# Optimization experiments

Hardware: AMD Instinct MI355X
Metric: run time of the kernel (lower is better)

Reference implementation:

```python
import jax, jax.numpy as jnp
import numpy as np

INPUT_DIM = 1024
OUTPUT_DIM = 1024
DEGREE = 8


def setup_inputs() -> dict:
    key = jax.random.key(0)
    k1, k2 = jax.random.split(key)
    x = jax.random.normal(k1, (8192, INPUT_DIM), dtype=jnp.float32)
    std = 1.0 / (INPUT_DIM * (DEGREE + 1))
    cheby_coeffs = jax.random.normal(k2, (INPUT_DIM, OUTPUT_DIM, DEGREE + 1), dtype=jnp.float32) * std
    return {"x": x, "cheby_coeffs": cheby_coeffs}


def reference(x, cheby_coeffs):
    # x: [B, I]; cheby_coeffs: [I, O, D+1]
    degree = cheby_coeffs.shape[-1] - 1
    t = jnp.clip(jnp.tanh(x), -0.999, 0.999)            # [B, I]
    theta = jnp.arccos(t)[..., None]                     # [B, I, 1]
    arange = jnp.arange(degree + 1, dtype=x.dtype)       # [D+1]
    basis = jnp.cos(theta * arange)                      # [B, I, D+1] Chebyshev T_d(t)
    y = jnp.einsum('bid,iod->bo', basis, cheby_coeffs)   # [B, O]
    return y
```

## Files before the change

### kernel.cpp

```cpp
#include <hip/hip_runtime.h>
#include <stdint.h>

#define B_ROWS 8192
#define I_DIM  1024
#define N_DIM  1024
#define NDEG   9
#define K_DIM  (I_DIM * (NDEG-1))

#define BM 256
#define BN 128
#define BK 64
#define NT (K_DIM / BK)

typedef __attribute__((ext_vector_type(8)))  short short8;
typedef __attribute__((ext_vector_type(16))) float f32x16;

__device__ __forceinline__ unsigned short f2bf(float f) {
  union { float f; uint32_t u; } v; v.f = f;
  uint32_t u = v.u;
  u += 0x7FFFu + ((u >> 16) & 1u);
  return (unsigned short)(u >> 16);
}

__device__ __forceinline__ float bf2f(unsigned short h) {
  union { uint32_t u; float f; } v; v.u = ((uint32_t)h) << 16;
  return v.f;
}

__device__ __forceinline__ uint32_t pk_bf16(float lo, float hi) {
  uint32_t r;
  asm("v_cvt_pk_bf16_f32 %0, %1, %2" : "=v"(r) : "v"(lo), "v"(hi));
  return r;
}

__device__ __forceinline__ float fast_tanh(float x) {
  float e = __expf(2.0f * x);
  return 1.0f - __fdividef(2.0f, e + 1.0f);
}

__device__ __forceinline__ int h2(int r) { return (r >> 2) & 7; }

__global__ __launch_bounds__(256) void repack_kernel(const float* __restrict__ cf,
                                                     unsigned short* __restrict__ Bt,
                                                     float* __restrict__ bias) {
  __shared__ unsigned short L[32][584];
  const int i0  = blockIdx.x * 32;
  const int o0  = blockIdx.y * 64;
  const int tid = threadIdx.x;

  #pragma unroll
  for (int j = 0; j < 18; ++j) {
    const int f4  = j * 256 + tid;
    const int il  = f4 / 144;
    const int odq = f4 % 144;
    const float4 v = *reinterpret_cast<const float4*>(
        cf + ((size_t)(i0 + il) * N_DIM + o0) * NDEG + (size_t)odq * 4);
    ushort4 w;
    w.x = f2bf(v.x); w.y = f2bf(v.y); w.z = f2bf(v.z); w.w = f2bf(v.w);
    *reinterpret_cast<ushort4*>(&L[il][odq * 4]) = w;
  }
  __syncthreads();

  const int o  = tid >> 2;
  const int ci = tid & 3;
  const size_t base = (size_t)(o0 + o) * K_DIM + (size_t)(i0 + ci * 8) * 8;
  #pragma unroll
  for (int p = 0; p < 8; ++p) {
    const int il = ci * 8 + p;
    uint4 u;
    u.x = (uint32_t)L[il][o*9 + 1] | ((uint32_t)L[il][o*9 + 2] << 16);
    u.y = (uint32_t)L[il][o*9 + 3] | ((uint32_t)L[il][o*9 + 4] << 16);
    u.z = (uint32_t)L[il][o*9 + 5] | ((uint32_t)L[il][o*9 + 6] << 16);
    u.w = (uint32_t)L[il][o*9 + 7] | ((uint32_t)L[il][o*9 + 8] << 16);
    *reinterpret_cast<uint4*>(Bt + base + (size_t)p * 8) = u;
  }
  if (tid < 64) {
    float s = 0.f;
    #pragma unroll
    for (int il = 0; il < 32; ++il) s += bf2f(L[il][tid * 9]);
    atomicAdd(&bias[o0 + tid], s);
  }
}

__global__ __launch_bounds__(512, 2) void gemm_kernel(const float* __restrict__ x,
                                                      const unsigned short* __restrict__ Bt,
                                                      const float* __restrict__ bias,
                                                      float* __restrict__ C) {
  extern __shared__ unsigned short sm[];
  const int tid  = threadIdx.x;
  const int lane = tid & 63;
  const int wave = tid >> 6;
  const int l31  = lane & 31;
  const int half = lane >> 5;
  const int wm   = wave >> 1;
  const int wn   = wave & 1;

  const int bid = blockIdx.x;
  const int mt  = (bid & 7) + 8 * (bid >> 6);
  const int nt  = (bid >> 3) & 7;
  const int m0  = mt * BM;
  const int n0  = nt * BN;

  const int sr   = tid >> 3;
  const int slot = tid & 7;

  const unsigned short* Bbase = Bt + (size_t)n0 * K_DIM;

  f32x16 acc[2][2];
  #pragma unroll
  for (int a = 0; a < 2; ++a)
    #pragma unroll
    for (int b = 0; b < 2; ++b)
      #pragma unroll
      for (int r = 0; r < 16; ++r)
        acc[a][b][r] = 0.f;

#define STAGE_B(s, bf, kk) { const int r_ = (s)*64 + sr; const int gc_ = slot ^ h2(r_);     \
    __builtin_amdgcn_global_load_lds(                                                       \
        (const __attribute__((address_space(1))) void*)(Bbase + (size_t)r_*K_DIM + (kk) + gc_*8), \
        (__attribute__((address_space(3))) void*)&sm[32768 + (bf)*8192 + r_*64 + slot*8], 16, 0, 0); }

#define LOADX(xr, tt) {                                                                     \
    _Pragma("unroll")                                                                       \
    for (int q = 0; q < 4; ++q)                                                             \
      xr[q] = x[(size_t)(m0 + q*64 + sr) * I_DIM + (tt)*8 + slot]; }

#define BASIS(bf, xr) {                                                                     \
    _Pragma("unroll")                                                                       \
    for (int q = 0; q < 4; ++q) {                                                           \
      const int r_ = q*64 + sr;                                                             \
      float t = fast_tanh(xr[q]);                                                           \
      t = fminf(fmaxf(t, -0.999f), 0.999f);                                                 \
      const float t2 = t + t;                                                               \
      const float T1 = t;                                                                   \
      const float T2 = t2*t - 1.0f;                                                         \
      const float T3 = t2*T2 - T1;                                                          \
      const float T4 = t2*T3 - T2;                                                          \
      const float T5 = t2*T4 - T3;                                                          \
      const float T6 = t2*T5 - T4;                                                          \
      const float T7 = t2*T6 - T5;                                                          \
      const float T8 = t2*T7 - T6;                                                          \
      uint4 u;                                                                              \
      u.x = pk_bf16(T1, T2); u.y = pk_bf16(T3, T4);                                         \
      u.z = pk_bf16(T5, T6); u.w = pk_bf16(T7, T8);                                         \
      *reinterpret_cast<uint4*>(&sm[(bf)*16384 + r_*64 + ((slot ^ h2(r_)))*8]) = u;         \
    } }

  { STAGE_B(0, 0, 0) STAGE_B(1, 0, 0) }
  float xr[4];
  LOADX(xr, 0)
  BASIS(0, xr)
  __syncthreads();

  const int rowA0 = wm * 64 + l31;
  const int rowA1 = wm * 64 + 32 + l31;
  const int rowB0 = wn * 64 + l31;
  const int rowB1 = wn * 64 + 32 + l31;
  const int hA0 = h2(rowA0), hA1 = h2(rowA1), hB0 = h2(rowB0), hB1 = h2(rowB1);

  for (int kt = 0; kt < NT; ++kt) {
    const int  cur  = kt & 1;
    const int  nxt  = cur ^ 1;
    const bool more = (kt + 1 < NT);
    const unsigned short* Asc = &sm[cur * 16384];
    const unsigned short* Bsc = &sm[32768 + cur * 8192];

    if (more) { STAGE_B(0, nxt, (kt + 1) * BK) STAGE_B(1, nxt, (kt + 1) * BK) LOADX(xr, kt + 1) }
    __builtin_amdgcn_sched_barrier(0);

    short8 av[2][4], bv[2][4];
#define READ4(ks) {                                                                          \
    const int c_ = (ks) * 2 + half;                                                          \
    av[0][ks] = *reinterpret_cast<const short8*>(&Asc[rowA0 * 64 + (c_ ^ hA0) * 8]);         \
    av[1][ks] = *reinterpret_cast<const short8*>(&Asc[rowA1 * 64 + (c_ ^ hA1) * 8]);         \
    bv[0][ks] = *reinterpret_cast<const short8*>(&Bsc[rowB0 * 64 + (c_ ^ hB0) * 8]);         \
    bv[1][ks] = *reinterpret_cast<const short8*>(&Bsc[rowB1 * 64 + (c_ ^ hB1) * 8]); }

    READ4(0)
    #pragma unroll
    for (int ks = 0; ks < 4; ++ks) {
      if (ks < 3) READ4(ks + 1)
      acc[0][0] = __builtin_amdgcn_mfma_f32_32x32x16_bf16(av[0][ks], bv[0][ks], acc[0][0], 0, 0, 0);
      acc[0][1] = __builtin_amdgcn_mfma_f32_32x32x16_bf16(av[0][ks], bv[1][ks], acc[0][1], 0, 0, 0);
      acc[1][0] = __builtin_amdgcn_mfma_f32_32x32x16_bf16(av[1][ks], bv[0][ks], acc[1][0], 0, 0, 0);
      acc[1][1] = __builtin_amdgcn_mfma_f32_32x32x16_bf16(av[1][ks], bv[1][ks], acc[1][1], 0, 0, 0);
      if (ks < 3) __builtin_amdgcn_sched_group_barrier(0x100, 4, 0);
      __builtin_amdgcn_sched_group_barrier(0x008, 4, 0);
    }
#undef READ4

    __builtin_amdgcn_sched_barrier(0);
    if (more) BASIS(nxt, xr)

    __syncthreads();
  }
#undef STAGE_B
#undef LOADX
#undef BASIS

  #pragma unroll
  for (int ni = 0; ni < 2; ++ni) {
    const int col  = n0 + wn * 64 + ni * 32 + l31;
    const float bc = bias[col];
    #pragma unroll
    for (int mi = 0; mi < 2; ++mi) {
      const int rbase = m0 + wm * 64 + mi * 32 + 4 * half;
      #pragma unroll
      for (int r = 0; r < 16; ++r) {
        const int row = rbase + (r & 3) + 8 * (r >> 2);
        C[(size_t)row * N_DIM + col] = acc[mi][ni][r] + bc;
      }
    }
  }
}

extern "C" void kernel_launch(void* const* d_in, const int* in_sizes, int n_in,
                              void* d_out, int out_size, void* d_ws, size_t ws_size,
                              hipStream_t stream) {
  const float* x      = (const float*)d_in[0];
  const float* coeffs = (const float*)d_in[1];
  float* y            = (float*)d_out;

  const size_t bt_bytes = (size_t)N_DIM * K_DIM * sizeof(unsigned short);
  unsigned short* Bt = (unsigned short*)d_ws;
  float* bias        = (float*)((char*)d_ws + bt_bytes);

  hipMemsetAsync(bias, 0, N_DIM * sizeof(float), stream);

  hipFuncSetAttribute((const void*)gemm_kernel,
                      hipFuncAttributeMaxDynamicSharedMemorySize, 98304);

  repack_kernel<<<dim3(I_DIM / 32, N_DIM / 64), 256, 0, stream>>>(coeffs, Bt, bias);
  gemm_kernel<<<(B_ROWS / BM) * (N_DIM / BN), 512, 98304, stream>>>(x, Bt, bias, y);
}
```

Baseline: 293.7 us.

## Interleave basis computation with MFMAs and prefetch x two tiles ahead

Restructures the main K loop: it is manually unrolled by two, and x values are double-buffered in registers and loaded two tiles ahead. The Chebyshev basis computation for the next A tile is split per row group and interleaved between the MFMA groups through sched_group_barrier, rather than run after all MFMAs. __syncthreads is replaced by explicit vmcnt/lgkmcnt waits plus s_barrier, and LDS write offsets and x pointers are precomputed. The aim is to hide the VALU basis math and global-load latency behind matrix ops, at the cost of more registers and fragile hand-written wait counts.

```diff
diff --git a/kernel.cpp b/kernel.cpp
--- a/kernel.cpp
+++ b/kernel.cpp
@@ -106,6 +106,15 @@
 
   const unsigned short* Bbase = Bt + (size_t)n0 * K_DIM;
 
+  int awoff[4];
+  const float* xptr[4];
+  #pragma unroll
+  for (int q = 0; q < 4; ++q) {
+    const int r_ = q * 64 + sr;
+    awoff[q] = r_ * 64 + (slot ^ h2(r_)) * 8;
+    xptr[q]  = x + (size_t)(m0 + r_) * I_DIM + slot;
+  }
+
   f32x16 acc[2][2];
   #pragma unroll
   for (int a = 0; a < 2; ++a)
@@ -122,14 +131,10 @@
 
 #define LOADX(xr, tt) {                                                                     \
     _Pragma("unroll")                                                                       \
-    for (int q = 0; q < 4; ++q)                                                             \
-      xr[q] = x[(size_t)(m0 + q*64 + sr) * I_DIM + (tt)*8 + slot]; }
-
-#define BASIS(bf, xr) {                                                                     \
-    _Pragma("unroll")                                                                       \
-    for (int q = 0; q < 4; ++q) {                                                           \
-      const int r_ = q*64 + sr;                                                             \
-      float t = fast_tanh(xr[q]);                                                           \
+    for (int q = 0; q < 4; ++q) xr[q] = xptr[q][(tt) * 8]; }
+
+#define BASIS_Q(bf, q, xv) {                                                                \
+      float t = fast_tanh(xv);                                                              \
       t = fminf(fmaxf(t, -0.999f), 0.999f);                                                 \
       const float t2 = t + t;                                                               \
       const float T1 = t;                                                                   \
@@ -143,14 +148,7 @@
       uint4 u;                                                                              \
       u.x = pk_bf16(T1, T2); u.y = pk_bf16(T3, T4);                                         \
       u.z = pk_bf16(T5, T6); u.w = pk_bf16(T7, T8);                                         \
-      *reinterpret_cast<uint4*>(&sm[(bf)*16384 + r_*64 + ((slot ^ h2(r_)))*8]) = u;         \
-    } }
-
-  { STAGE_B(0, 0, 0) STAGE_B(1, 0, 0) }
-  float xr[4];
-  LOADX(xr, 0)
-  BASIS(0, xr)
-  __syncthreads();
+      *reinterpret_cast<uint4*>(&sm[(bf)*16384 + awoff[q]]) = u; }
 
   const int rowA0 = wm * 64 + l31;
   const int rowA1 = wm * 64 + 32 + l31;
@@ -158,45 +156,91 @@
   const int rowB1 = wn * 64 + 32 + l31;
   const int hA0 = h2(rowA0), hA1 = h2(rowA1), hB0 = h2(rowB0), hB1 = h2(rowB1);
 
-  for (int kt = 0; kt < NT; ++kt) {
-    const int  cur  = kt & 1;
-    const int  nxt  = cur ^ 1;
-    const bool more = (kt + 1 < NT);
-    const unsigned short* Asc = &sm[cur * 16384];
-    const unsigned short* Bsc = &sm[32768 + cur * 8192];
-
-    if (more) { STAGE_B(0, nxt, (kt + 1) * BK) STAGE_B(1, nxt, (kt + 1) * BK) LOADX(xr, kt + 1) }
-    __builtin_amdgcn_sched_barrier(0);
-
-    short8 av[2][4], bv[2][4];
-#define READ4(ks) {                                                                          \
+#define READ4(Asc, Bsc, av, bv, ks) {                                                        \
     const int c_ = (ks) * 2 + half;                                                          \
     av[0][ks] = *reinterpret_cast<const short8*>(&Asc[rowA0 * 64 + (c_ ^ hA0) * 8]);         \
     av[1][ks] = *reinterpret_cast<const short8*>(&Asc[rowA1 * 64 + (c_ ^ hA1) * 8]);         \
     bv[0][ks] = *reinterpret_cast<const short8*>(&Bsc[rowB0 * 64 + (c_ ^ hB0) * 8]);         \
     bv[1][ks] = *reinterpret_cast<const short8*>(&Bsc[rowB1 * 64 + (c_ ^ hB1) * 8]); }
 
-    READ4(0)
+#define MFMA4(av, bv, ks)                                                                    \
+    acc[0][0] = __builtin_amdgcn_mfma_f32_32x32x16_bf16(av[0][ks], bv[0][ks], acc[0][0], 0, 0, 0); \
+    acc[0][1] = __builtin_amdgcn_mfma_f32_32x32x16_bf16(av[0][ks], bv[1][ks], acc[0][1], 0, 0, 0); \
+    acc[1][0] = __builtin_amdgcn_mfma_f32_32x32x16_bf16(av[1][ks], bv[0][ks], acc[1][0], 0, 0, 0); \
+    acc[1][1] = __builtin_amdgcn_mfma_f32_32x32x16_bf16(av[1][ks], bv[1][ks], acc[1][1], 0, 0, 0);
+
+#define TILE_FULL(kt_, XC, XL, LOADEN) {                                                     \
+    const int cur_ = (kt_) & 1; const int nxt_ = cur_ ^ 1;                                   \
+    const unsigned short* Asc = &sm[cur_ * 16384];                                           \
+    const unsigned short* Bsc = &sm[32768 + cur_ * 8192];                                    \
+    STAGE_B(0, nxt_, ((kt_) + 1) * BK) STAGE_B(1, nxt_, ((kt_) + 1) * BK)                    \
+    if (LOADEN) { LOADX(XL, (kt_) + 2) }                                                     \
+    __builtin_amdgcn_sched_barrier(0);                                                       \
+    short8 av[2][4], bv[2][4];                                                               \
+    READ4(Asc, Bsc, av, bv, 0)                                                               \
+    READ4(Asc, Bsc, av, bv, 1)                                                               \
+    BASIS_Q(nxt_, 0, XC[0])                                                                  \
+    MFMA4(av, bv, 0)                                                                         \
+    __builtin_amdgcn_sched_group_barrier(0x100, 8, 0);                                       \
+    __builtin_amdgcn_sched_group_barrier(0x200, 1, 0);                                       \
+    __builtin_amdgcn_sched_group_barrier(0x008, 4, 0);                                       \
+    READ4(Asc, Bsc, av, bv, 2)                                                               \
+    BASIS_Q(nxt_, 1, XC[1])                                                                  \
+    MFMA4(av, bv, 1)                                                                         \
+    __builtin_amdgcn_sched_group_barrier(0x100, 4, 0);                                       \
+    __builtin_amdgcn_sched_group_barrier(0x200, 1, 0);                                       \
+    __builtin_amdgcn_sched_group_barrier(0x008, 4, 0);                                       \
+    READ4(Asc, Bsc, av, bv, 3)                                                               \
+    BASIS_Q(nxt_, 2, XC[2])                                                                  \
+    MFMA4(av, bv, 2)                                                                         \
+    __builtin_amdgcn_sched_group_barrier(0x100, 4, 0);                                       \
+    __builtin_amdgcn_sched_group_barrier(0x200, 1, 0);                                       \
+    __builtin_amdgcn_sched_group_barrier(0x008, 4, 0);                                       \
+    BASIS_Q(nxt_, 3, XC[3])                                                                  \
+    MFMA4(av, bv, 3)                                                                         \
+    __builtin_amdgcn_sched_group_barrier(0x200, 1, 0);                                       \
+    __builtin_amdgcn_sched_group_barrier(0x008, 4, 0);                                       \
+    __builtin_amdgcn_sched_barrier(0);                                                       \
+    if (LOADEN) asm volatile("s_waitcnt vmcnt(4) lgkmcnt(0)" ::: "memory");                  \
+    else        asm volatile("s_waitcnt vmcnt(0) lgkmcnt(0)" ::: "memory");                  \
+    __builtin_amdgcn_s_barrier();                                                            \
+    __builtin_amdgcn_sched_barrier(0); }
+
+  float xrA[4], xrB[4];
+  STAGE_B(0, 0, 0) STAGE_B(1, 0, 0)
+  LOADX(xrA, 0)
+  LOADX(xrB, 1)
+  asm volatile("s_waitcnt vmcnt(4)" ::: "memory");
+  BASIS_Q(0, 0, xrA[0]) BASIS_Q(0, 1, xrA[1]) BASIS_Q(0, 2, xrA[2]) BASIS_Q(0, 3, xrA[3])
+  asm volatile("s_waitcnt lgkmcnt(0)" ::: "memory");
+  __builtin_amdgcn_s_barrier();
+  __builtin_amdgcn_sched_barrier(0);
+
+  for (int kt = 0; kt < 126; kt += 2) {
+    TILE_FULL(kt,     xrB, xrA, 1)
+    TILE_FULL(kt + 1, xrA, xrB, 1)
+  }
+  TILE_FULL(126, xrB, xrA, 0)
+
+  {
+    const unsigned short* Asc = &sm[1 * 16384];
+    const unsigned short* Bsc = &sm[32768 + 1 * 8192];
+    short8 av[2][4], bv[2][4];
+    READ4(Asc, Bsc, av, bv, 0)
     #pragma unroll
     for (int ks = 0; ks < 4; ++ks) {
-      if (ks < 3) READ4(ks + 1)
-      acc[0][0] = __builtin_amdgcn_mfma_f32_32x32x16_bf16(av[0][ks], bv[0][ks], acc[0][0], 0, 0, 0);
-      acc[0][1] = __builtin_amdgcn_mfma_f32_32x32x16_bf16(av[0][ks], bv[1][ks], acc[0][1], 0, 0, 0);
-      acc[1][0] = __builtin_amdgcn_mfma_f32_32x32x16_bf16(av[1][ks], bv[0][ks], acc[1][0], 0, 0, 0);
-      acc[1][1] = __builtin_amdgcn_mfma_f32_32x32x16_bf16(av[1][ks], bv[1][ks], acc[1][1], 0, 0, 0);
+      if (ks < 3) READ4(Asc, Bsc, av, bv, ks + 1)
+      MFMA4(av, bv, ks)
       if (ks < 3) __builtin_amdgcn_sched_group_barrier(0x100, 4, 0);
       __builtin_amdgcn_sched_group_barrier(0x008, 4, 0);
     }
+  }
+#undef TILE_FULL
+#undef MFMA4
 #undef READ4
-
-    __builtin_amdgcn_sched_barrier(0);
-    if (more) BASIS(nxt, xr)
-
-    __syncthreads();
-  }
+#undef BASIS_Q
+#undef LOADX
 #undef STAGE_B
-#undef LOADX
-#undef BASIS
 
   #pragma unroll
   for (int ni = 0; ni < 2; ++ni) {
```

After: 256.0 us. 12.9% less time.

## Warp-specialize GEMM with producer waves computing basis and staging B

Applied to the files above, without the earlier changes.

Splits the GEMM block into 8 consumer waves running MFMA and 4 producer waves that load x, compute the Chebyshev basis into LDS and stage pre-tiled B via global_load_lds. The repack kernel now writes B in an MFMA-fragment-ordered layout, so LDS reads need no XOR swizzle and B staging is contiguous. The goal is to overlap basis computation and loads with the matrix math instead of running them serially inside each wave. In exchange the block grows to 768 threads with launch bounds of 3, which raises register pressure. Synchronization now relies on hand-placed barriers and waitcnts, where a mismatch would be a correctness risk.

```diff
diff --git a/kernel.cpp b/kernel.cpp
--- a/kernel.cpp
+++ b/kernel.cpp
@@ -38,10 +38,8 @@
   return 1.0f - __fdividef(2.0f, e + 1.0f);
 }
 
-__device__ __forceinline__ int h2(int r) { return (r >> 2) & 7; }
-
 __global__ __launch_bounds__(256) void repack_kernel(const float* __restrict__ cf,
-                                                     unsigned short* __restrict__ Bt,
+                                                     unsigned short* __restrict__ Bt2,
                                                      float* __restrict__ bias) {
   __shared__ unsigned short L[32][584];
   const int i0  = blockIdx.x * 32;
@@ -61,18 +59,23 @@
   }
   __syncthreads();
 
-  const int o  = tid >> 2;
-  const int ci = tid & 3;
-  const size_t base = (size_t)(o0 + o) * K_DIM + (size_t)(i0 + ci * 8) * 8;
+  const int o_rel = tid >> 2;
+  const int ci    = tid & 3;
+  const int o     = o0 + o_rel;
+  const int ntb   = o >> 7;
+  const int gb    = (o & 127) >> 5;
+  const int r31   = o & 31;
+  const int kti   = (i0 >> 3) + ci;
+  const size_t base = (size_t)ntb * 1048576 + (size_t)kti * 8192 + (size_t)r31 * 8;
   #pragma unroll
   for (int p = 0; p < 8; ++p) {
     const int il = ci * 8 + p;
     uint4 u;
-    u.x = (uint32_t)L[il][o*9 + 1] | ((uint32_t)L[il][o*9 + 2] << 16);
-    u.y = (uint32_t)L[il][o*9 + 3] | ((uint32_t)L[il][o*9 + 4] << 16);
-    u.z = (uint32_t)L[il][o*9 + 5] | ((uint32_t)L[il][o*9 + 6] << 16);
-    u.w = (uint32_t)L[il][o*9 + 7] | ((uint32_t)L[il][o*9 + 8] << 16);
-    *reinterpret_cast<uint4*>(Bt + base + (size_t)p * 8) = u;
+    u.x = (uint32_t)L[il][o_rel*9 + 1] | ((uint32_t)L[il][o_rel*9 + 2] << 16);
+    u.y = (uint32_t)L[il][o_rel*9 + 3] | ((uint32_t)L[il][o_rel*9 + 4] << 16);
+    u.z = (uint32_t)L[il][o_rel*9 + 5] | ((uint32_t)L[il][o_rel*9 + 6] << 16);
+    u.w = (uint32_t)L[il][o_rel*9 + 7] | ((uint32_t)L[il][o_rel*9 + 8] << 16);
+    *reinterpret_cast<uint4*>(Bt2 + base + (size_t)(gb * 8 + p) * 256) = u;
   }
   if (tid < 64) {
     float s = 0.f;
@@ -82,18 +85,13 @@
   }
 }
 
-__global__ __launch_bounds__(512, 2) void gemm_kernel(const float* __restrict__ x,
-                                                      const unsigned short* __restrict__ Bt,
+__global__ __launch_bounds__(768, 3) void gemm_kernel(const float* __restrict__ x,
+                                                      const unsigned short* __restrict__ Bt2,
                                                       const float* __restrict__ bias,
                                                       float* __restrict__ C) {
   extern __shared__ unsigned short sm[];
   const int tid  = threadIdx.x;
-  const int lane = tid & 63;
   const int wave = tid >> 6;
-  const int l31  = lane & 31;
-  const int half = lane >> 5;
-  const int wm   = wave >> 1;
-  const int wn   = wave & 1;
 
   const int bid = blockIdx.x;
   const int mt  = (bid & 7) + 8 * (bid >> 6);
@@ -101,116 +99,154 @@
   const int m0  = mt * BM;
   const int n0  = nt * BN;
 
-  const int sr   = tid >> 3;
-  const int slot = tid & 7;
-
-  const unsigned short* Bbase = Bt + (size_t)n0 * K_DIM;
-
-  f32x16 acc[2][2];
-  #pragma unroll
-  for (int a = 0; a < 2; ++a)
+  if (wave < 8) {
+    const int lane = tid & 63;
+    const int l31  = lane & 31;
+    const int half = lane >> 5;
+    const int wm   = wave >> 1;
+    const int wn   = wave & 1;
+
+    const int aoff0 = ((wm * 2 + 0) * 8 + half) * 256 + l31 * 8;
+    const int aoff1 = ((wm * 2 + 1) * 8 + half) * 256 + l31 * 8;
+    const int boff0 = ((wn * 2 + 0) * 8 + half) * 256 + l31 * 8;
+    const int boff1 = ((wn * 2 + 1) * 8 + half) * 256 + l31 * 8;
+
+    f32x16 acc[2][2];
     #pragma unroll
-    for (int b = 0; b < 2; ++b)
+    for (int a = 0; a < 2; ++a)
       #pragma unroll
-      for (int r = 0; r < 16; ++r)
-        acc[a][b][r] = 0.f;
-
-#define STAGE_B(s, bf, kk) { const int r_ = (s)*64 + sr; const int gc_ = slot ^ h2(r_);     \
-    __builtin_amdgcn_global_load_lds(                                                       \
-        (const __attribute__((address_space(1))) void*)(Bbase + (size_t)r_*K_DIM + (kk) + gc_*8), \
-        (__attribute__((address_space(3))) void*)&sm[32768 + (bf)*8192 + r_*64 + slot*8], 16, 0, 0); }
-
-#define LOADX(xr, tt) {                                                                     \
-    _Pragma("unroll")                                                                       \
-    for (int q = 0; q < 4; ++q)                                                             \
-      xr[q] = x[(size_t)(m0 + q*64 + sr) * I_DIM + (tt)*8 + slot]; }
-
-#define BASIS(bf, xr) {                                                                     \
-    _Pragma("unroll")                                                                       \
-    for (int q = 0; q < 4; ++q) {                                                           \
-      const int r_ = q*64 + sr;                                                             \
-      float t = fast_tanh(xr[q]);                                                           \
-      t = fminf(fmaxf(t, -0.999f), 0.999f);                                                 \
-      const float t2 = t + t;                                                               \
-      const float T1 = t;                                                                   \
-      const float T2 = t2*t - 1.0f;                                                         \
-      const float T3 = t2*T2 - T1;                                                          \
-      const float T4 = t2*T3 - T2;                                                          \
-      const float T5 = t2*T4 - T3;                                                          \
-      const float T6 = t2*T5 - T4;                                                          \
-      const float T7 = t2*T6 - T5;                                                          \
-      const float T8 = t2*T7 - T6;                                                          \
-      uint4 u;                                                                              \
-      u.x = pk_bf16(T1, T2); u.y = pk_bf16(T3, T4);                                         \
-      u.z = pk_bf16(T5, T6); u.w = pk_bf16(T7, T8);                                         \
-      *reinterpret_cast<uint4*>(&sm[(bf)*16384 + r_*64 + ((slot ^ h2(r_)))*8]) = u;         \
-    } }
-
-  { STAGE_B(0, 0, 0) STAGE_B(1, 0, 0) }
-  float xr[4];
-  LOADX(xr, 0)
-  BASIS(0, xr)
-  __syncthreads();
-
-  const int rowA0 = wm * 64 + l31;
-  const int rowA1 = wm * 64 + 32 + l31;
-  const int rowB0 = wn * 64 + l31;
-  const int rowB1 = wn * 64 + 32 + l31;
-  const int hA0 = h2(rowA0), hA1 = h2(rowA1), hB0 = h2(rowB0), hB1 = h2(rowB1);
-
-  for (int kt = 0; kt < NT; ++kt) {
-    const int  cur  = kt & 1;
-    const int  nxt  = cur ^ 1;
-    const bool more = (kt + 1 < NT);
-    const unsigned short* Asc = &sm[cur * 16384];
-    const unsigned short* Bsc = &sm[32768 + cur * 8192];
-
-    if (more) { STAGE_B(0, nxt, (kt + 1) * BK) STAGE_B(1, nxt, (kt + 1) * BK) LOADX(xr, kt + 1) }
-    __builtin_amdgcn_sched_barrier(0);
+      for (int b = 0; b < 2; ++b)
+        #pragma unroll
+        for (int r = 0; r < 16; ++r)
+          acc[a][b][r] = 0.f;
 
     short8 av[2][4], bv[2][4];
-#define READ4(ks) {                                                                          \
-    const int c_ = (ks) * 2 + half;                                                          \
-    av[0][ks] = *reinterpret_cast<const short8*>(&Asc[rowA0 * 64 + (c_ ^ hA0) * 8]);         \
-    av[1][ks] = *reinterpret_cast<const short8*>(&Asc[rowA1 * 64 + (c_ ^ hA1) * 8]);         \
-    bv[0][ks] = *reinterpret_cast<const short8*>(&Bsc[rowB0 * 64 + (c_ ^ hB0) * 8]);         \
-    bv[1][ks] = *reinterpret_cast<const short8*>(&Bsc[rowB1 * 64 + (c_ ^ hB1) * 8]); }
-
-    READ4(0)
+
+#define READ4(As_, Bs_, ks) {                                                                \
+    av[0][ks] = *reinterpret_cast<const short8*>(&(As_)[aoff0 + (ks) * 512]);                \
+    av[1][ks] = *reinterpret_cast<const short8*>(&(As_)[aoff1 + (ks) * 512]);                \
+    bv[0][ks] = *reinterpret_cast<const short8*>(&(Bs_)[boff0 + (ks) * 512]);                \
+    bv[1][ks] = *reinterpret_cast<const short8*>(&(Bs_)[boff1 + (ks) * 512]); }
+
+#define MFMA4(ks)                                                                            \
+    acc[0][0] = __builtin_amdgcn_mfma_f32_32x32x16_bf16(av[0][ks], bv[0][ks], acc[0][0], 0, 0, 0); \
+    acc[0][1] = __builtin_amdgcn_mfma_f32_32x32x16_bf16(av[0][ks], bv[1][ks], acc[0][1], 0, 0, 0); \
+    acc[1][0] = __builtin_amdgcn_mfma_f32_32x32x16_bf16(av[1][ks], bv[0][ks], acc[1][0], 0, 0, 0); \
+    acc[1][1] = __builtin_amdgcn_mfma_f32_32x32x16_bf16(av[1][ks], bv[1][ks], acc[1][1], 0, 0, 0);
+
+#define CPIN { __builtin_amdgcn_sched_group_barrier(0x100, 4, 0);                            \
+               __builtin_amdgcn_sched_group_barrier(0x008, 4, 0); }
+
+#define CTILE(bufsel) {                                                                      \
+    const unsigned short* As_ = &sm[(bufsel) * 16384];                                       \
+    const unsigned short* Bs_ = &sm[32768 + (bufsel) * 8192];                                \
+    READ4(As_, Bs_, 0)                                                                       \
+    READ4(As_, Bs_, 1) MFMA4(0) CPIN                                                         \
+    READ4(As_, Bs_, 2) MFMA4(1) CPIN                                                         \
+    READ4(As_, Bs_, 3) MFMA4(2) CPIN                                                         \
+    MFMA4(3) __builtin_amdgcn_sched_group_barrier(0x008, 4, 0); }
+
+#define CBAR { __builtin_amdgcn_sched_barrier(0); __builtin_amdgcn_s_barrier();              \
+               __builtin_amdgcn_sched_barrier(0); }
+
+    CBAR
+    for (int kt = 0; kt < 126; kt += 2) {
+      CTILE(0) CBAR
+      CTILE(1) CBAR
+    }
+    CTILE(0) CBAR
+    CTILE(1)
+#undef CTILE
+#undef CPIN
+#undef READ4
+
     #pragma unroll
-    for (int ks = 0; ks < 4; ++ks) {
-      if (ks < 3) READ4(ks + 1)
-      acc[0][0] = __builtin_amdgcn_mfma_f32_32x32x16_bf16(av[0][ks], bv[0][ks], acc[0][0], 0, 0, 0);
-      acc[0][1] = __builtin_amdgcn_mfma_f32_32x32x16_bf16(av[0][ks], bv[1][ks], acc[0][1], 0, 0, 0);
-      acc[1][0] = __builtin_amdgcn_mfma_f32_32x32x16_bf16(av[1][ks], bv[0][ks], acc[1][0], 0, 0, 0);
-      acc[1][1] = __builtin_amdgcn_mfma_f32_32x32x16_bf16(av[1][ks], bv[1][ks], acc[1][1], 0, 0, 0);
-      if (ks < 3) __builtin_amdgcn_sched_group_barrier(0x100, 4, 0);
-      __builtin_amdgcn_sched_group_barrier(0x008, 4, 0);
-    }
-#undef READ4
-
-    __builtin_amdgcn_sched_barrier(0);
-    if (more) BASIS(nxt, xr)
-
-    __syncthreads();
-  }
-#undef STAGE_B
-#undef LOADX
-#undef BASIS
-
-  #pragma unroll
-  for (int ni = 0; ni < 2; ++ni) {
-    const int col  = n0 + wn * 64 + ni * 32 + l31;
-    const float bc = bias[col];
-    #pragma unroll
-    for (int mi = 0; mi < 2; ++mi) {
-      const int rbase = m0 + wm * 64 + mi * 32 + 4 * half;
+    for (int ni = 0; ni < 2; ++ni) {
+      const int col  = n0 + wn * 64 + ni * 32 + l31;
+      const float bc = bias[col];
       #pragma unroll
-      for (int r = 0; r < 16; ++r) {
-        const int row = rbase + (r & 3) + 8 * (r >> 2);
-        C[(size_t)row * N_DIM + col] = acc[mi][ni][r] + bc;
+      for (int mi = 0; mi < 2; ++mi) {
+        const int rbase = m0 + wm * 64 + mi * 32 + 4 * half;
+        #pragma unroll
+        for (int r = 0; r < 16; ++r) {
+          const int row = rbase + (r & 3) + 8 * (r >> 2);
+          C[(size_t)row * N_DIM + col] = acc[mi][ni][r] + bc;
+        }
       }
     }
+#undef MFMA4
+#undef CBAR
+  } else {
+    const int pr = tid - 512;
+    const float* xrow = x + (size_t)(m0 + pr) * I_DIM;
+    const unsigned short* BtSlab = Bt2 + (size_t)nt * 1048576;
+    const int awbase = (pr >> 5) * 2048 + (pr & 31) * 8;
+    const int prw8   = pr * 8;
+
+#define STAGEB(bufsel, kt1) {                                                                \
+    _Pragma("unroll")                                                                        \
+    for (int q = 0; q < 4; ++q) {                                                            \
+      __builtin_amdgcn_global_load_lds(                                                      \
+        (const __attribute__((address_space(1))) void*)(BtSlab + (size_t)(kt1) * 8192 + q * 2048 + prw8), \
+        (__attribute__((address_space(3))) void*)&sm[32768 + (bufsel) * 8192 + q * 2048 + prw8], 16, 0, 0); \
+    } }
+
+#define BASIS8(bufsel, f0, f1) {                                                             \
+    const float tin[8] = {(f0).x, (f0).y, (f0).z, (f0).w, (f1).x, (f1).y, (f1).z, (f1).w};   \
+    _Pragma("unroll")                                                                        \
+    for (int s = 0; s < 8; ++s) {                                                            \
+      float t = fast_tanh(tin[s]);                                                           \
+      t = fminf(fmaxf(t, -0.999f), 0.999f);                                                  \
+      const float t2 = t + t;                                                                \
+      const float T1 = t;                                                                    \
+      const float T2 = t2 * t - 1.0f;                                                        \
+      const float T3 = t2 * T2 - T1;                                                         \
+      const float T4 = t2 * T3 - T2;                                                         \
+      const float T5 = t2 * T4 - T3;                                                         \
+      const float T6 = t2 * T5 - T4;                                                         \
+      const float T7 = t2 * T6 - T5;                                                         \
+      const float T8 = t2 * T7 - T6;                                                         \
+      uint4 u;                                                                               \
+      u.x = pk_bf16(T1, T2); u.y = pk_bf16(T3, T4);                                          \
+      u.z = pk_bf16(T5, T6); u.w = pk_bf16(T7, T8);                                          \
+      *reinterpret_cast<uint4*>(&sm[(bufsel) * 16384 + awbase + s * 256]) = u;               \
+    } }
+
+    float4 xE0, xE1, xO0, xO1;
+    xE0 = *reinterpret_cast<const float4*>(xrow + 0);
+    xE1 = *reinterpret_cast<const float4*>(xrow + 4);
+    xO0 = *reinterpret_cast<const float4*>(xrow + 8);
+    xO1 = *reinterpret_cast<const float4*>(xrow + 12);
+    STAGEB(0, 0)
+    BASIS8(0, xE0, xE1)
+    __builtin_amdgcn_sched_barrier(0);
+    asm volatile("s_waitcnt vmcnt(0) lgkmcnt(0)" ::: "memory");
+    __builtin_amdgcn_s_barrier();
+    __builtin_amdgcn_sched_barrier(0);
+
+#define PTILE(kt_, XU0, XU1, XL0, XL1, LX) {                                                 \
+    STAGEB(((kt_) + 1) & 1, (kt_) + 1)                                                       \
+    __builtin_amdgcn_sched_barrier(0);                                                       \
+    BASIS8(((kt_) + 1) & 1, XU0, XU1)                                                        \
+    __builtin_amdgcn_sched_barrier(0);                                                       \
+    if (LX) {                                                                                \
+      XL0 = *reinterpret_cast<const float4*>(xrow + ((kt_) + 2) * 8);                        \
+      XL1 = *reinterpret_cast<const float4*>(xrow + ((kt_) + 2) * 8 + 4);                    \
+    }                                                                                        \
+    __builtin_amdgcn_sched_barrier(0);                                                       \
+    if (LX) { asm volatile("s_waitcnt vmcnt(2) lgkmcnt(0)" ::: "memory"); }                  \
+    else    { asm volatile("s_waitcnt vmcnt(0) lgkmcnt(0)" ::: "memory"); }                  \
+    __builtin_amdgcn_s_barrier();                                                            \
+    __builtin_amdgcn_sched_barrier(0); }
+
+    for (int kt = 0; kt < 126; kt += 2) {
+      PTILE(kt,     xO0, xO1, xE0, xE1, 1)
+      PTILE(kt + 1, xE0, xE1, xO0, xO1, 1)
+    }
+    PTILE(126, xO0, xO1, xE0, xE1, 0)
+#undef PTILE
+#undef BASIS8
+#undef STAGEB
   }
 }
 
@@ -222,14 +258,14 @@
   float* y            = (float*)d_out;
 
   const size_t bt_bytes = (size_t)N_DIM * K_DIM * sizeof(unsigned short);
-  unsigned short* Bt = (unsigned short*)d_ws;
-  float* bias        = (float*)((char*)d_ws + bt_bytes);
+  unsigned short* Bt2 = (unsigned short*)d_ws;
+  float* bias         = (float*)((char*)d_ws + bt_bytes);
 
   hipMemsetAsync(bias, 0, N_DIM * sizeof(float), stream);
 
   hipFuncSetAttribute((const void*)gemm_kernel,
                       hipFuncAttributeMaxDynamicSharedMemorySize, 98304);
 
-  repack_kernel<<<dim3(I_DIM / 32, N_DIM / 64), 256, 0, stream>>>(coeffs, Bt, bias);
-  gemm_kernel<<<(B_ROWS / BM) * (N_DIM / BN), 512, 98304, stream>>>(x, Bt, bias, y);
-}
+  repack_kernel<<<dim3(I_DIM / 32, N_DIM / 64), 256, 0, stream>>>(coeffs, Bt2, bias);
+  gemm_kernel<<<(B_ROWS / BM) * (N_DIM / BN), 768, 98304, stream>>>(x, Bt2, bias, y);
+}
```

Result: faster. 266.3 us (-9.4%).
